# Kernel tuning notes

Hardware: AMD Instinct MI355X
Metric: run time of the kernel (lower is better)

Reference implementation:

```python
import jax, jax.numpy as jnp
import numpy as np
from jax import lax

D = 384      # embd_d
L = 4        # num_blocks
B = 64
SHW, THW = 24, 12
NS, NT = SHW * SHW, THW * THW   # 576, 144
EPS = 1e-5


def _ln(x, g, b):
    mu = jnp.mean(x, axis=-1, keepdims=True)
    var = jnp.mean(jnp.square(x - mu), axis=-1, keepdims=True)
    return (x - mu) * lax.rsqrt(var + EPS) * g + b


def setup_inputs() -> dict:
    key = jax.random.key(0)
    ks = iter(jax.random.split(key, 64))
    f32 = jnp.float32
    def nrm(shape, s=0.02):
        return jax.random.normal(next(ks), shape, dtype=f32) * s
    inp = {
        'search': jax.random.normal(next(ks), (B, NS, D), dtype=f32),
        'target': jax.random.normal(next(ks), (B, NT, D), dtype=f32),
        # learned tokens / positional params
        'cls': nrm((1, 1, D), 1.0),
        'search_pos': nrm((1, NS, D), 0.5),
        'target_pos': nrm((1, NT, D), 0.5),
        # stacked per-block params [L, ...]
        'ln1_g': jnp.ones((L, D), f32), 'ln1_b': jnp.zeros((L, D), f32),
        'Wq': nrm((L, D, D)), 'bq': jnp.zeros((L, D), f32),
        'Wk': nrm((L, D, D)), 'bk': jnp.zeros((L, D), f32),
        'Wv': nrm((L, D, D)), 'bv': jnp.zeros((L, D), f32),
        'ln2_g': jnp.ones((L, D), f32), 'ln2_b': jnp.zeros((L, D), f32),
        'W1': nrm((L, D, 2 * D)), 'b1': jnp.zeros((L, 2 * D), f32),
        'W2': nrm((L, 2 * D, D)), 'b2': jnp.zeros((L, D), f32),
        # head
        'lnf_g': jnp.ones((D,), f32), 'lnf_b': jnp.zeros((D,), f32),
        'Wl1': nrm((D, D)), 'bl1': jnp.zeros((D,), f32),
        'Wl2': nrm((D, 1)), 'bl2': jnp.zeros((1,), f32),
    }
    return inp


def reference(search, target, cls, search_pos, target_pos,
              ln1_g, ln1_b, Wq, bq, Wk, bk, Wv, bv,
              ln2_g, ln2_b, W1, b1, W2, b2,
              lnf_g, lnf_b, Wl1, bl1, Wl2, bl2):
    scale = D ** (-0.5)  # note: full embed dim, as in source
    x = jnp.concatenate([
        jnp.broadcast_to(cls, (B, 1, D)),
        search + search_pos,
        target + target_pos,
    ], axis=1)  # [B, 1+Ns+Nt, D]

    def block(x, p):
        l1g, l1b, wq, bq_, wk, bk_, wv, bv_, l2g, l2b, w1, b1_, w2, b2_ = p
        y = _ln(x, l1g, l1b)
        q = y @ wq + bq_
        k = y @ wk + bk_
        v = y @ wv + bv_
        attn = jax.nn.softmax(jnp.einsum('bid,bjd->bij', q, k) * scale, axis=-1)
        x = x + jnp.einsum('bij,bjd->bid', attn, v)
        h = _ln(x, l2g, l2b)
        x = x + (jax.nn.gelu(h @ w1 + b1_, approximate=False) @ w2 + b2_)
        return x, None

    x, _ = lax.scan(block, x, (ln1_g, ln1_b, Wq, bq, Wk, bk, Wv, bv,
                               ln2_g, ln2_b, W1, b1, W2, b2))
    h = _ln(x[:, 0], lnf_g, lnf_b)          # cls token [B, D]
    h = jax.nn.relu(h @ Wl1 + bl1)
    return h @ Wl2 + bl2                     # [B, 1]
```

## Files before the change

### kernel.cpp

```cpp
#include <hip/hip_runtime.h>
#include <hip/hip_bf16.h>
#include <math.h>

#define DD 384
#define NBATCH 64
#define NSEQ 721
#define NROWS (NBATCH*NSEQ)
#define NLAYER 4
#define VTW 736

typedef __bf16 bf16_t;
typedef __bf16 bf16x8 __attribute__((ext_vector_type(8)));
typedef float  f32x4  __attribute__((ext_vector_type(4)));

static __device__ __forceinline__ void split_bf16(float v, bf16_t& h, bf16_t& l) {
    h = (bf16_t)v;
    l = (bf16_t)(v - (float)h);
}
static __device__ __forceinline__ bf16x8 bzero8() {
    bf16x8 v = {(bf16_t)0.f,(bf16_t)0.f,(bf16_t)0.f,(bf16_t)0.f,
                (bf16_t)0.f,(bf16_t)0.f,(bf16_t)0.f,(bf16_t)0.f};
    return v;
}
static __device__ __forceinline__ void gload16(const void* g, void* l) {
    __builtin_amdgcn_global_load_lds(
        (const __attribute__((address_space(1))) unsigned int*)g,
        (__attribute__((address_space(3))) unsigned int*)l, 16, 0, 0);
}
static __device__ __forceinline__ int xcd_swz(int nwg) {
    int orig = blockIdx.x;
    int q = nwg >> 3, r = nwg & 7;
    int xcd = orig & 7, within = orig >> 3;
    int base = (xcd < r) ? xcd*(q+1) : r*(q+1) + (xcd - r)*q;
    return base + within;
}
static __device__ __forceinline__ void ln_from_partials(const float* ss, const float* ss2,
                                                        int row, float& mu, float& rstd) {
    float s = 0.f, q2 = 0.f;
    #pragma unroll
    for (int k = 0; k < 6; ++k) { s += ss[k*NROWS + row]; q2 += ss2[k*NROWS + row]; }
    mu = s * (1.f/DD);
    float var = q2 * (1.f/DD) - mu*mu;
    rstd = rsqrtf(var + 1e-5f);
}

__global__ __launch_bounds__(256) void build_x_kernel(const float* __restrict__ search,
                               const float* __restrict__ target,
                               const float* __restrict__ cls,
                               const float* __restrict__ spos,
                               const float* __restrict__ tpos,
                               bf16_t* __restrict__ xh, bf16_t* __restrict__ xl,
                               float* __restrict__ wss, float* __restrict__ wss2) {
    int wave = threadIdx.x >> 6, lane = threadIdx.x & 63;
    int row = blockIdx.x * 4 + wave;
    if (row >= NROWS) return;
    int b = row / NSEQ, n = row % NSEQ;
    float s = 0.f, q2 = 0.f;
    #pragma unroll
    for (int i = 0; i < 6; ++i) {
        int d = lane + 64*i;
        float val;
        if (n == 0)        val = cls[d];
        else if (n <= 576) val = search[((size_t)b*576 + (n-1))*DD + d] + spos[(size_t)(n-1)*DD + d];
        else               val = target[((size_t)b*144 + (n-577))*DD + d] + tpos[(size_t)(n-577)*DD + d];
        bf16_t h, l;
        split_bf16(val, h, l);
        xh[(size_t)row*DD + d] = h;
        xl[(size_t)row*DD + d] = l;
        s += val; q2 += val*val;
    }
    #pragma unroll
    for (int m = 1; m < 64; m <<= 1) { s += __shfl_xor(s, m); q2 += __shfl_xor(q2, m); }
    if (lane == 0) {
        wss[row] = s; wss2[row] = q2;
        #pragma unroll
        for (int k = 1; k < 6; ++k) { wss[k*NROWS + row] = 0.f; wss2[k*NROWS + row] = 0.f; }
    }
}

__global__ void transpose_split_kernel(const float* __restrict__ src,
                                       const float* __restrict__ g,
                                       bf16_t* __restrict__ dh,
                                       bf16_t* __restrict__ dl,
                                       int K, int N) {
    int idx = blockIdx.x * blockDim.x + threadIdx.x;
    if (idx >= K*N) return;
    int k = idx / N, n = idx % N;
    float v = src[idx];
    if (g) v *= g[k];
    bf16_t h, l;
    split_bf16(v, h, l);
    dh[(size_t)n*K + k] = h;
    dl[(size_t)n*K + k] = l;
}

__global__ void colsum_kernel(const float* __restrict__ W, const float* __restrict__ g,
                              const float* __restrict__ b, const float* __restrict__ bias,
                              float* __restrict__ c1, float* __restrict__ c2,
                              int K, int N, int outStride, int outOff) {
    int l = blockIdx.y;
    int n = blockIdx.x * 256 + threadIdx.x;
    if (n >= N) return;
    const float* Wl = W + (size_t)l*K*N;
    const float* gl = g + (size_t)l*K;
    const float* bl = b + (size_t)l*K;
    float s1 = 0.f, s2 = 0.f;
    for (int k = 0; k < K; ++k) {
        float w = Wl[(size_t)k*N + n];
        s1 = fmaf(gl[k], w, s1);
        s2 = fmaf(bl[k], w, s2);
    }
    c1[(size_t)l*outStride + outOff + n] = s1;
    c2[(size_t)l*outStride + outOff + n] = s2 + bias[(size_t)l*N + n];
}

static __device__ __forceinline__ void gemm_core(
        const bf16_t* __restrict__ ah, const bf16_t* __restrict__ al,
        const bf16_t* __restrict__ bh, const bf16_t* __restrict__ bl,
        bf16_t (&ls)[32][64][8],
        int m0, int n0, int K, f32x4 (&acc)[4][4]) {
    int t = threadIdx.x;
    int w = t >> 6, lane = t & 63;
    int c = lane & 15, g = lane >> 4;
    int wr = w >> 1, wc = w & 1;
    const bf16_t* src0 = (w==0) ? ah : (w==1) ? al : (w==2) ? bh : bl;
    int base_rc = (w < 2) ? m0 : n0;
    const bf16_t* srcbase = src0 + (size_t)(base_rc + c)*K + 8*g;

    int ksteps = K >> 5;
    for (int kt = 0; kt < ksteps; ++kt) {
        int k0 = kt << 5;
        __syncthreads();
        #pragma unroll
        for (int i = 0; i < 8; ++i)
            gload16(srcbase + (size_t)(16*i)*K + k0, &ls[w*8 + i][0][0]);
        __syncthreads();
        bf16x8 af_h[4], af_l[4], bf_h[4], bf_l[4];
        #pragma unroll
        for (int i = 0; i < 4; ++i) {
            af_h[i] = *(const bf16x8*)&ls[     4*wr + i][lane][0];
            af_l[i] = *(const bf16x8*)&ls[ 8 + 4*wr + i][lane][0];
            bf_h[i] = *(const bf16x8*)&ls[16 + 4*wc + i][lane][0];
            bf_l[i] = *(const bf16x8*)&ls[24 + 4*wc + i][lane][0];
        }
        #pragma unroll
        for (int i = 0; i < 4; ++i)
            #pragma unroll
            for (int j = 0; j < 4; ++j) {
                acc[i][j] = __builtin_amdgcn_mfma_f32_16x16x32_bf16(af_h[i], bf_h[j], acc[i][j], 0,0,0);
                acc[i][j] = __builtin_amdgcn_mfma_f32_16x16x32_bf16(af_h[i], bf_l[j], acc[i][j], 0,0,0);
                acc[i][j] = __builtin_amdgcn_mfma_f32_16x16x32_bf16(af_l[i], bf_h[j], acc[i][j], 0,0,0);
            }
    }
}

__global__ __launch_bounds__(256, 4) void gemm_qkv(
        const bf16_t* __restrict__ ah, const bf16_t* __restrict__ al,
        const bf16_t* __restrict__ bh, const bf16_t* __restrict__ bl,
        const float* __restrict__ ss, const float* __restrict__ ss2,
        const float* __restrict__ c1, const float* __restrict__ c2,
        bf16_t* __restrict__ qout, bf16_t* __restrict__ kout,
        bf16_t* __restrict__ vth,
        int nwg) {
    __shared__ __align__(16) bf16_t ls[32][64][8];
    int wgid = xcd_swz(nwg);
    int mt = wgid / 9, n0 = (wgid % 9) * 128;
    int blb = mt / 6;
    int tok_base = (mt % 6) * 128;
    int m0d = blb*NSEQ + tok_base;
    f32x4 zero4 = {0.f,0.f,0.f,0.f};
    f32x4 acc[4][4];
    #pragma unroll
    for (int i = 0; i < 4; ++i)
        #pragma unroll
        for (int j = 0; j < 4; ++j) acc[i][j] = zero4;
    gemm_core(ah, al, bh, bl, ls, m0d, n0, DD, acc);

    int t = threadIdx.x, w = t >> 6, lane = t & 63;
    int c = lane & 15, g = lane >> 4;
    int wr = w >> 1, wc = w & 1;
    float rmu[16], rrs[16];
    #pragma unroll
    for (int i = 0; i < 4; ++i)
        #pragma unroll
        for (int r = 0; r < 4; ++r) {
            int tok = tok_base + 64*wr + 16*i + 4*g + r;
            float mu = 0.f, rstd = 1.f;
            if (tok < NSEQ) ln_from_partials(ss, ss2, blb*NSEQ + tok, mu, rstd);
            rmu[i*4+r] = mu; rrs[i*4+r] = rstd;
        }
    int seg = n0 / 384;
    bf16_t* LST = &ls[0][0][0];
    if (seg < 2) {
        bf16_t* outb = (seg == 0) ? qout : kout;
        int segoff = seg * 384;
        __syncthreads();
        #pragma unroll
        for (int j = 0; j < 4; ++j) {
            int nl = 64*wc + 16*j + c;
            float C1 = c1[n0 + nl], C2 = c2[n0 + nl];
            #pragma unroll
            for (int i = 0; i < 4; ++i)
                #pragma unroll
                for (int r = 0; r < 4; ++r) {
                    int rl = 64*wr + 16*i + 4*g + r;
                    float val = rrs[i*4+r]*(acc[i][j][r] - rmu[i*4+r]*C1) + C2;
                    LST[rl*128 + (nl ^ ((rl & 15) << 3))] = (bf16_t)val;
                }
        }
        __syncthreads();
        #pragma unroll
        for (int p = 0; p < 8; ++p) {
            int chunk = t + 256*p;
            int rl = chunk >> 4;
            int nl0 = (chunk & 15) * 8;
            int tok = tok_base + rl;
            if (tok >= NSEQ) continue;
            uint4 v = *(const uint4*)&LST[rl*128 + (nl0 ^ ((rl & 15) << 3))];
            *(uint4*)(outb + (size_t)(blb*NSEQ + tok)*DD + (n0 - segoff) + nl0) = v;
        }
    } else {
        int vbase = n0 - 768;
        __syncthreads();
        #pragma unroll
        for (int j = 0; j < 4; ++j) {
            int d = 64*wc + 16*j + c;
            float C1 = c1[n0 + d], C2 = c2[n0 + d];
            #pragma unroll
            for (int i = 0; i < 4; ++i)
                #pragma unroll
                for (int r = 0; r < 4; ++r) {
                    int tokl = 64*wr + 16*i + 4*g + r;
                    float val = rrs[i*4+r]*(acc[i][j][r] - rmu[i*4+r]*C1) + C2;
                    if (tok_base + tokl >= NSEQ) val = 0.f;
                    LST[d*128 + (tokl ^ ((d & 15) << 3))] = (bf16_t)val;
                }
        }
        __syncthreads();
        #pragma unroll
        for (int p = 0; p < 8; ++p) {
            int chunk = t + 256*p;
            int d = chunk >> 4;
            int tok0 = (chunk & 15) * 8;
            int tg = tok_base + tok0;
            if (tg + 8 > VTW) continue;
            uint4 v = *(const uint4*)&LST[d*128 + (tok0 ^ ((d & 15) << 3))];
            *(uint4*)(vth + ((size_t)(blb*DD + vbase + d))*VTW + tg) = v;
        }
    }
}

template<int EPI, int NT>
__global__ __launch_bounds__(256, 4) void gemm_mfma(
        const bf16_t* __restrict__ ah, const bf16_t* __restrict__ al,
        const bf16_t* __restrict__ bh, const bf16_t* __restrict__ bl,
        const float* __restrict__ ss, const float* __restrict__ ss2,
        const float* __restrict__ c1, const float* __restrict__ c2,
        const float* __restrict__ bias,
        const bf16_t* __restrict__ resh, const bf16_t* __restrict__ resl,
        bf16_t* __restrict__ o1, bf16_t* __restrict__ o2,
        float* __restrict__ wss, float* __restrict__ wss2,
        int M, int N, int K, int nwg) {
    __shared__ __align__(16) bf16_t ls[32][64][8];
    int wgid = xcd_swz(nwg);
    int m0 = (wgid / NT) * 128, n0 = (wgid % NT) * 128;
    f32x4 zero4 = {0.f,0.f,0.f,0.f};
    f32x4 acc[4][4];
    #pragma unroll
    for (int i = 0; i < 4; ++i)
        #pragma unroll
        for (int j = 0; j < 4; ++j) acc[i][j] = zero4;
    gemm_core(ah, al, bh, bl, ls, m0, n0, K, acc);

    int t = threadIdx.x, w = t >> 6, lane = t & 63;
    int c = lane & 15, g = lane >> 4;
    int wr = w >> 1, wc = w & 1;

    if (EPI == 2) {
        float rmu[16], rrs[16];
        #pragma unroll
        for (int i = 0; i < 4; ++i)
            #pragma unroll
            for (int r = 0; r < 4; ++r) {
                int row = m0 + 64*wr + 16*i + 4*g + r;
                float mu = 0.f, rstd = 1.f;
                if (row < M) ln_from_partials(ss, ss2, row, mu, rstd);
                rmu[i*4+r] = mu; rrs[i*4+r] = rstd;
            }
        #pragma unroll
        for (int j = 0; j < 4; ++j) {
            int n = n0 + 64*wc + 16*j + c;
            float C1 = c1[n], C2 = c2[n];
            #pragma unroll
            for (int i = 0; i < 4; ++i) {
                int rbase = m0 + 64*wr + 16*i + 4*g;
                #pragma unroll
                for (int r = 0; r < 4; ++r) {
                    int row = rbase + r;
                    if (row >= M) continue;
                    float val = rrs[i*4+r]*(acc[i][j][r] - rmu[i*4+r]*C1) + C2;
                    val = 0.5f*val*(1.0f + erff(val*0.70710678118654752f));
                    bf16_t h, l;
                    split_bf16(val, h, l);
                    size_t o = (size_t)row*N + n;
                    o1[o] = h;
                    o2[o] = l;
                }
            }
        }
    } else {
        int slot = (wgid % NT) + 3*wc;
        #pragma unroll
        for (int i = 0; i < 4; ++i)
            #pragma unroll
            for (int r = 0; r < 4; ++r) {
                int row = m0 + 64*wr + 16*i + 4*g + r;
                if (row >= M) continue;
                float s = 0.f, q2 = 0.f;
                #pragma unroll
                for (int j = 0; j < 4; ++j) {
                    int n = n0 + 64*wc + 16*j + c;
                    size_t o = (size_t)row*N + n;
                    float val = acc[i][j][r] + bias[n] + (float)resh[o] + (float)resl[o];
                    bf16_t h, l;
                    split_bf16(val, h, l);
                    o1[o] = h;
                    o2[o] = l;
                    s += val; q2 += val*val;
                }
                #pragma unroll
                for (int m = 1; m < 16; m <<= 1) { s += __shfl_xor(s, m); q2 += __shfl_xor(q2, m); }
                if (c == 0) {
                    wss[slot*NROWS + row] = s;
                    wss2[slot*NROWS + row] = q2;
                }
            }
    }
}

__global__ __launch_bounds__(256, 2) void attn_mfma(
        const bf16_t* __restrict__ qh, const bf16_t* __restrict__ kh,
        const bf16_t* __restrict__ vth,
        bf16_t* __restrict__ xh, bf16_t* __restrict__ xl,
        float* __restrict__ wss, float* __restrict__ wss2, int nwg) {
    __shared__ __align__(16) char smem[49152];
    bf16_t* kf = (bf16_t*)smem;
    char* vhp = smem + 24576;

    int t = threadIdx.x, w = t >> 6, lane = t & 63;
    int c = lane & 15, g = lane >> 4;
    int wgid = xcd_swz(nwg);
    int bl_ = wgid / 12;
    int q0 = (wgid % 12) * 64;
    size_t bb = (size_t)bl_ * NSEQ;
    int qrow = q0 + 16*w + c;
    bool qok = (qrow < NSEQ);
    const float scale = 0.05103103630798287f;
    int vswz = (c ^ (c >> 2)) & 3;
    int dma_dd  = lane >> 2;
    int dma_kv8 = (lane & 3) ^ ((dma_dd ^ (dma_dd >> 2)) & 3);

    bf16x8 qf[12];
    #pragma unroll
    for (int ks = 0; ks < 12; ++ks) {
        if (qok) qf[ks] = *(const bf16x8*)(qh + (bb + qrow)*DD + 32*ks + 8*g);
        else     qf[ks] = bzero8();
    }

    f32x4 zero4 = {0.f,0.f,0.f,0.f};
    f32x4 oacc[24];
    #pragma unroll
    for (int i = 0; i < 24; ++i) oacc[i] = zero4;
    float m_run = -1e30f, l_run = 0.f;

    #pragma unroll
    for (int i = 0; i < 6; ++i) {
        int s = i*4 + w;
        int ks = s >> 1, mf = s & 1;
        gload16(kh + (bb + (size_t)(16*mf + c))*DD + 32*ks + 8*g, kf + s*512);
    }

    for (int kt = 0; kt < 23; ++kt) {
        int kv0 = kt * 32;
        asm volatile("s_waitcnt vmcnt(0)" ::: "memory");
        __builtin_amdgcn_s_barrier();
        #pragma unroll
        for (int i = 0; i < 6; ++i) {
            int s = i*4 + w;
            size_t gro = ((size_t)(bl_*DD + 16*s + dma_dd))*VTW + kv0 + 8*dma_kv8;
            gload16(vth + gro, (bf16_t*)vhp + s*512);
        }
        f32x4 sacc[2];
        sacc[0] = zero4; sacc[1] = zero4;
        #pragma unroll
        for (int ks = 0; ks < 12; ++ks) {
            bf16x8 a0 = *(const bf16x8*)(kf + ((size_t)(2*ks+0)*64 + lane)*8);
            bf16x8 a1 = *(const bf16x8*)(kf + ((size_t)(2*ks+1)*64 + lane)*8);
            sacc[0] = __builtin_amdgcn_mfma_f32_16x16x32_bf16(a0, qf[ks], sacc[0], 0,0,0);
            sacc[1] = __builtin_amdgcn_mfma_f32_16x16x32_bf16(a1, qf[ks], sacc[1], 0,0,0);
        }
        float p[2][4];
        float mx = -1e30f;
        #pragma unroll
        for (int mf = 0; mf < 2; ++mf)
            #pragma unroll
            for (int r = 0; r < 4; ++r) {
                float sv = sacc[mf][r] * scale;
                int kv = kv0 + 16*mf + 4*g + r;
                if (kv >= NSEQ) sv = -1e30f;
                p[mf][r] = sv;
                mx = fmaxf(mx, sv);
            }
        mx = fmaxf(mx, __shfl_xor(mx, 16));
        mx = fmaxf(mx, __shfl_xor(mx, 32));
        bool skip = __all(mx <= m_run + 8.f);
        float m_new = skip ? m_run : fmaxf(m_run, mx);
        float psum = 0.f;
        #pragma unroll
        for (int mf = 0; mf < 2; ++mf)
            #pragma unroll
            for (int r = 0; r < 4; ++r) {
                float pv = __expf(p[mf][r] - m_new);
                p[mf][r] = pv;
                psum += pv;
            }
        psum += __shfl_xor(psum, 16);
        psum += __shfl_xor(psum, 32);
        if (!skip) {
            float corr = __expf(m_run - m_new);
            l_run = l_run * corr + psum;
            #pragma unroll
            for (int i = 0; i < 24; ++i) oacc[i] *= corr;
            m_run = m_new;
        } else {
            l_run += psum;
        }
        bf16x8 ph, pl;
        #pragma unroll
        for (int mf = 0; mf < 2; ++mf)
            #pragma unroll
            for (int r = 0; r < 4; ++r) {
                bf16_t hh, ll;
                split_bf16(p[mf][r], hh, ll);
                ph[mf*4 + r] = hh;
                pl[mf*4 + r] = ll;
            }
        asm volatile("s_waitcnt vmcnt(0)" ::: "memory");
        __builtin_amdgcn_s_barrier();
        if (kt + 1 < 23) {
            int kv0n = kv0 + 32;
            #pragma unroll
            for (int i = 0; i < 6; ++i) {
                int s = i*4 + w;
                int ks = s >> 1, mf = s & 1;
                gload16(kh + (bb + (size_t)(kv0n + 16*mf + c))*DD + 32*ks + 8*g, kf + s*512);
            }
        }
        #pragma unroll
        for (int mf = 0; mf < 24; ++mf) {
            int dr = 16*mf + c;
            const char* vb = vhp + dr*64;
            int o0 = ((((g>>1)     ^ vswz) << 4) | (8*(g&1)));
            int o1 = (((2 + (g>>1)) ^ vswz) << 4) | (8*(g&1));
            union { uint2 u[2]; bf16x8 v; } va;
            va.u[0] = *(const uint2*)(vb + o0);
            va.u[1] = *(const uint2*)(vb + o1);
            oacc[mf] = __builtin_amdgcn_mfma_f32_16x16x32_bf16(va.v, ph, oacc[mf], 0,0,0);
            oacc[mf] = __builtin_amdgcn_mfma_f32_16x16x32_bf16(va.v, pl, oacc[mf], 0,0,0);
        }
    }
    float inv = 1.f / l_run;
    float s = 0.f, q2 = 0.f;
    if (qok) {
        bf16_t* xhr = xh + (bb + qrow)*DD;
        bf16_t* xlr = xl + (bb + qrow)*DD;
        #pragma unroll
        for (int mf = 0; mf < 24; ++mf)
            #pragma unroll
            for (int r = 0; r < 4; ++r) {
                int d = 16*mf + 4*g + r;
                float xv = (float)xhr[d] + (float)xlr[d] + oacc[mf][r]*inv;
                bf16_t h, l;
                split_bf16(xv, h, l);
                xhr[d] = h;
                xlr[d] = l;
                s += xv; q2 += xv*xv;
            }
    }
    s += __shfl_xor(s, 16);  q2 += __shfl_xor(q2, 16);
    s += __shfl_xor(s, 32);  q2 += __shfl_xor(q2, 32);
    if (qok && g == 0) {
        int rowL = bl_*NSEQ + qrow;
        wss[rowL] = s; wss2[rowL] = q2;
        #pragma unroll
        for (int k = 1; k < 6; ++k) { wss[k*NROWS + rowL] = 0.f; wss2[k*NROWS + rowL] = 0.f; }
    }
}

__global__ __launch_bounds__(384) void head_kernel(const bf16_t* __restrict__ xh,
    const bf16_t* __restrict__ xl,
    const float* __restrict__ g, const float* __restrict__ bb,
    const float* __restrict__ Wl1, const float* __restrict__ bl1,
    const float* __restrict__ Wl2, const float* __restrict__ bl2,
    float* __restrict__ outp) {
    __shared__ float yv[384];
    __shared__ float r1[6], r2[6], r3[6];
    int b = blockIdx.x, t = threadIdx.x;
    size_t o = (size_t)b*NSEQ*DD + t;
    float v = (float)xh[o] + (float)xl[o];
    float s = v;
    #pragma unroll
    for (int m = 1; m < 64; m <<= 1) s += __shfl_xor(s, m);
    if ((t & 63) == 0) r1[t>>6] = s;
    __syncthreads();
    float mu = (r1[0]+r1[1]+r1[2]+r1[3]+r1[4]+r1[5]) * (1.f/384.f);
    float dd = v - mu;
    float sq = dd*dd;
    #pragma unroll
    for (int m = 1; m < 64; m <<= 1) sq += __shfl_xor(sq, m);
    if ((t & 63) == 0) r2[t>>6] = sq;
    __syncthreads();
    float var = (r2[0]+r2[1]+r2[2]+r2[3]+r2[4]+r2[5]) * (1.f/384.f);
    float rstd = rsqrtf(var + 1e-5f);
    yv[t] = dd*rstd*g[t] + bb[t];
    __syncthreads();
    float acc = bl1[t];
    for (int d2 = 0; d2 < 384; d2++) acc = fmaf(yv[d2], Wl1[d2*384 + t], acc);
    acc = fmaxf(acc, 0.f);
    float oo = acc * Wl2[t];
    #pragma unroll
    for (int m = 1; m < 64; m <<= 1) oo += __shfl_xor(oo, m);
    if ((t & 63) == 0) r3[t>>6] = oo;
    __syncthreads();
    if (t == 0) outp[b] = r3[0]+r3[1]+r3[2]+r3[3]+r3[4]+r3[5] + bl2[0];
}

extern "C" void kernel_launch(void* const* d_in, const int* in_sizes, int n_in,
                              void* d_out, int out_size, void* d_ws, size_t ws_size,
                              hipStream_t stream) {
    const float* search = (const float*)d_in[0];
    const float* target = (const float*)d_in[1];
    const float* cls    = (const float*)d_in[2];
    const float* spos   = (const float*)d_in[3];
    const float* tpos   = (const float*)d_in[4];
    const float* ln1_g  = (const float*)d_in[5];
    const float* ln1_b  = (const float*)d_in[6];
    const float* Wq     = (const float*)d_in[7];
    const float* bq     = (const float*)d_in[8];
    const float* Wk     = (const float*)d_in[9];
    const float* bk     = (const float*)d_in[10];
    const float* Wv     = (const float*)d_in[11];
    const float* bv     = (const float*)d_in[12];
    const float* ln2_g  = (const float*)d_in[13];
    const float* ln2_b  = (const float*)d_in[14];
    const float* W1     = (const float*)d_in[15];
    const float* b1     = (const float*)d_in[16];
    const float* W2     = (const float*)d_in[17];
    const float* b2     = (const float*)d_in[18];
    const float* lnf_g  = (const float*)d_in[19];
    const float* lnf_b  = (const float*)d_in[20];
    const float* Wl1    = (const float*)d_in[21];
    const float* bl1    = (const float*)d_in[22];
    const float* Wl2    = (const float*)d_in[23];
    const float* bl2    = (const float*)d_in[24];

    size_t off = 0;
    char* base = (char*)d_ws;
    auto alloc = [&](size_t bytes) -> void* {
        void* p = base + off;
        off += (bytes + 255) & ~(size_t)255;
        return p;
    };

    bf16_t* xh = (bf16_t*)alloc((size_t)NROWS * DD * 2);
    bf16_t* xl = (bf16_t*)alloc((size_t)NROWS * DD * 2);
    float* ssum  = (float*)alloc((size_t)6*NROWS*4);
    float* ssum2 = (float*)alloc((size_t)6*NROWS*4);

    const int SQKV = 1152*DD;
    const int SM = DD*768;
    bf16_t* wqkvh = (bf16_t*)alloc((size_t)4*SQKV*2);
    bf16_t* wqkvl = (bf16_t*)alloc((size_t)4*SQKV*2);
    bf16_t* w1h = (bf16_t*)alloc((size_t)4*SM*2);
    bf16_t* w1l = (bf16_t*)alloc((size_t)4*SM*2);
    bf16_t* w2h = (bf16_t*)alloc((size_t)4*SM*2);
    bf16_t* w2l = (bf16_t*)alloc((size_t)4*SM*2);
    float* cqkv1 = (float*)alloc((size_t)4*1152*4);
    float* cqkv2 = (float*)alloc((size_t)4*1152*4);
    float* cm11  = (float*)alloc((size_t)4*768*4);
    float* cm12  = (float*)alloc((size_t)4*768*4);

    const size_t qB  = (size_t)NSEQ*DD*2;
    const size_t mB  = (size_t)NSEQ*768*2;
    const size_t perB = 2*mB;
    size_t avail = (ws_size > off + 262144) ? (ws_size - off - 262144) : 0;
    int G = (int)(avail / perB);
    if (G > NBATCH) G = NBATCH;
    if (G < 1) G = 1;

    char* U = (char*)alloc(perB * G);
    bf16_t* qhB  = (bf16_t*)U;
    bf16_t* khB  = (bf16_t*)(U + qB*G);
    bf16_t* vth  = (bf16_t*)(U + 2*qB*G);
    bf16_t* midh = (bf16_t*)U;
    bf16_t* midl = (bf16_t*)(U + mB*G);

    build_x_kernel<<<(NROWS+3)/4, 256, 0, stream>>>(search, target, cls, spos, tpos,
                                                    xh, xl, ssum, ssum2);

    const int SQ = DD*DD;
    for (int l = 0; l < NLAYER; ++l) {
        bf16_t* dsth = wqkvh + (size_t)l*SQKV;
        bf16_t* dstl = wqkvl + (size_t)l*SQKV;
        transpose_split_kernel<<<(SQ+255)/256, 256, 0, stream>>>(Wq + (size_t)l*SQ, ln1_g + l*DD, dsth,          dstl,          DD, DD);
        transpose_split_kernel<<<(SQ+255)/256, 256, 0, stream>>>(Wk + (size_t)l*SQ, ln1_g + l*DD, dsth + 384*DD, dstl + 384*DD, DD, DD);
        transpose_split_kernel<<<(SQ+255)/256, 256, 0, stream>>>(Wv + (size_t)l*SQ, ln1_g + l*DD, dsth + 768*DD, dstl + 768*DD, DD, DD);
        transpose_split_kernel<<<(SM+255)/256, 256, 0, stream>>>(W1 + (size_t)l*SM, ln2_g + l*DD, w1h + (size_t)l*SM, w1l + (size_t)l*SM, DD, 768);
        transpose_split_kernel<<<(SM+255)/256, 256, 0, stream>>>(W2 + (size_t)l*SM, nullptr,      w2h + (size_t)l*SM, w2l + (size_t)l*SM, 768, DD);
    }
    colsum_kernel<<<dim3(2, NLAYER), 256, 0, stream>>>(Wq, ln1_g, ln1_b, bq, cqkv1, cqkv2, DD, DD, 1152, 0);
    colsum_kernel<<<dim3(2, NLAYER), 256, 0, stream>>>(Wk, ln1_g, ln1_b, bk, cqkv1, cqkv2, DD, DD, 1152, 384);
    colsum_kernel<<<dim3(2, NLAYER), 256, 0, stream>>>(Wv, ln1_g, ln1_b, bv, cqkv1, cqkv2, DD, DD, 1152, 768);
    colsum_kernel<<<dim3(3, NLAYER), 256, 0, stream>>>(W1, ln2_g, ln2_b, b1, cm11, cm12, DD, 768, 768, 0);

    for (int l = 0; l < NLAYER; ++l) {
        for (int b0 = 0; b0 < NBATCH; b0 += G) {
            int cb = (NBATCH - b0 < G) ? (NBATCH - b0) : G;
            int Mc = cb * NSEQ;
            bf16_t* xch = xh + (size_t)b0 * NSEQ * DD;
            bf16_t* xcl = xl + (size_t)b0 * NSEQ * DD;
            float* ssc  = ssum  + (size_t)b0 * NSEQ;
            float* ssc2 = ssum2 + (size_t)b0 * NSEQ;
            int mtiles = (Mc + 127)/128;
            int nwgQKV = 9*6*cb, nwgM1 = 6*mtiles, nwgM2 = 3*mtiles, nwgA = 12*cb;

            gemm_qkv<<<nwgQKV, 256, 0, stream>>>(xch, xcl,
                    wqkvh + (size_t)l*SQKV, wqkvl + (size_t)l*SQKV,
                    ssc, ssc2, cqkv1 + l*1152, cqkv2 + l*1152,
                    qhB, khB, vth, nwgQKV);
            attn_mfma<<<nwgA, 256, 0, stream>>>(qhB, khB, vth, xch, xcl,
                    ssc, ssc2, nwgA);
            gemm_mfma<2,6><<<nwgM1, 256, 0, stream>>>(xch, xcl,
                    w1h + (size_t)l*SM, w1l + (size_t)l*SM,
                    ssc, ssc2, cm11 + l*768, cm12 + l*768, nullptr,
                    nullptr, nullptr, midh, midl, nullptr, nullptr, Mc, 768, DD, nwgM1);
            gemm_mfma<3,3><<<nwgM2, 256, 0, stream>>>(midh, midl,
                    w2h + (size_t)l*SM, w2l + (size_t)l*SM,
                    nullptr, nullptr, nullptr, nullptr, b2 + l*DD,
                    xch, xcl, xch, xcl, ssc, ssc2, Mc, DD, 768, nwgM2);
        }
    }
    head_kernel<<<NBATCH, 384, 0, stream>>>(xh, xl, lnf_g, lnf_b, Wl1, bl1, Wl2, bl2, (float*)d_out);
}
```

Measured before the change: 3.237 ms.

## Drop activation low-part MFMAs in QKV/MLP1 and stage epilogue stores through LDS

```diff
diff --git a/kernel.cpp b/kernel.cpp
--- a/kernel.cpp
+++ b/kernel.cpp
@@ -114,7 +114,7 @@
     c2[(size_t)l*outStride + outOff + n] = s2 + bias[(size_t)l*N + n];
 }
 
-static __device__ __forceinline__ void gemm_core(
+static __device__ __forceinline__ void gemm_core3(
         const bf16_t* __restrict__ ah, const bf16_t* __restrict__ al,
         const bf16_t* __restrict__ bh, const bf16_t* __restrict__ bl,
         bf16_t (&ls)[32][64][8],
@@ -154,8 +154,48 @@
     }
 }
 
+static __device__ __forceinline__ void gemm_core2(
+        const bf16_t* __restrict__ ah,
+        const bf16_t* __restrict__ bh, const bf16_t* __restrict__ bl,
+        bf16_t (&ls)[32][64][8],
+        int m0, int n0, int K, f32x4 (&acc)[4][4]) {
+    int t = threadIdx.x;
+    int w = t >> 6, lane = t & 63;
+    int c = lane & 15, g = lane >> 4;
+    int wr = w >> 1, wc = w & 1;
+
+    int ksteps = K >> 5;
+    for (int kt = 0; kt < ksteps; ++kt) {
+        int k0 = kt << 5;
+        __syncthreads();
+        #pragma unroll
+        for (int i = 0; i < 6; ++i) {
+            int s = w*6 + i;
+            const bf16_t* src = (s < 8) ? ah : (s < 16) ? bh : bl;
+            int base = (s < 8) ? m0 : n0;
+            int row = base + (s & 7)*16 + c;
+            gload16(src + (size_t)row*K + k0 + 8*g, &ls[s][0][0]);
+        }
+        __syncthreads();
+        bf16x8 af[4], bfh[4], bfl[4];
+        #pragma unroll
+        for (int i = 0; i < 4; ++i) {
+            af[i]  = *(const bf16x8*)&ls[     4*wr + i][lane][0];
+            bfh[i] = *(const bf16x8*)&ls[ 8 + 4*wc + i][lane][0];
+            bfl[i] = *(const bf16x8*)&ls[16 + 4*wc + i][lane][0];
+        }
+        #pragma unroll
+        for (int i = 0; i < 4; ++i)
+            #pragma unroll
+            for (int j = 0; j < 4; ++j) {
+                acc[i][j] = __builtin_amdgcn_mfma_f32_16x16x32_bf16(af[i], bfh[j], acc[i][j], 0,0,0);
+                acc[i][j] = __builtin_amdgcn_mfma_f32_16x16x32_bf16(af[i], bfl[j], acc[i][j], 0,0,0);
+            }
+    }
+}
+
 __global__ __launch_bounds__(256, 4) void gemm_qkv(
-        const bf16_t* __restrict__ ah, const bf16_t* __restrict__ al,
+        const bf16_t* __restrict__ ah,
         const bf16_t* __restrict__ bh, const bf16_t* __restrict__ bl,
         const float* __restrict__ ss, const float* __restrict__ ss2,
         const float* __restrict__ c1, const float* __restrict__ c2,
@@ -174,7 +214,7 @@
     for (int i = 0; i < 4; ++i)
         #pragma unroll
         for (int j = 0; j < 4; ++j) acc[i][j] = zero4;
-    gemm_core(ah, al, bh, bl, ls, m0d, n0, DD, acc);
+    gemm_core2(ah, bh, bl, ls, m0d, n0, DD, acc);
 
     int t = threadIdx.x, w = t >> 6, lane = t & 63;
     int c = lane & 15, g = lane >> 4;
@@ -250,91 +290,179 @@
     }
 }
 
-template<int EPI, int NT>
-__global__ __launch_bounds__(256, 4) void gemm_mfma(
-        const bf16_t* __restrict__ ah, const bf16_t* __restrict__ al,
+__global__ __launch_bounds__(256, 4) void gemm_m1(
+        const bf16_t* __restrict__ ah,
         const bf16_t* __restrict__ bh, const bf16_t* __restrict__ bl,
         const float* __restrict__ ss, const float* __restrict__ ss2,
         const float* __restrict__ c1, const float* __restrict__ c2,
+        bf16_t* __restrict__ o1, bf16_t* __restrict__ o2,
+        int M, int nwg) {
+    __shared__ __align__(16) bf16_t ls[32][64][8];
+    int wgid = xcd_swz(nwg);
+    int m0 = (wgid / 6) * 128, n0 = (wgid % 6) * 128;
+    f32x4 zero4 = {0.f,0.f,0.f,0.f};
+    f32x4 acc[4][4];
+    #pragma unroll
+    for (int i = 0; i < 4; ++i)
+        #pragma unroll
+        for (int j = 0; j < 4; ++j) acc[i][j] = zero4;
+    gemm_core2(ah, bh, bl, ls, m0, n0, DD, acc);
+
+    int t = threadIdx.x, w = t >> 6, lane = t & 63;
+    int c = lane & 15, g = lane >> 4;
+    int wr = w >> 1, wc = w & 1;
+    float rmu[16], rrs[16];
+    #pragma unroll
+    for (int i = 0; i < 4; ++i)
+        #pragma unroll
+        for (int r = 0; r < 4; ++r) {
+            int row = m0 + 64*wr + 16*i + 4*g + r;
+            float mu = 0.f, rstd = 1.f;
+            if (row < M) ln_from_partials(ss, ss2, row, mu, rstd);
+            rmu[i*4+r] = mu; rrs[i*4+r] = rstd;
+        }
+    bf16_t* LST = &ls[0][0][0];
+    __syncthreads();
+    #pragma unroll
+    for (int j = 0; j < 4; ++j) {
+        int nl = 64*wc + 16*j + c;
+        float C1 = c1[n0 + nl], C2 = c2[n0 + nl];
+        #pragma unroll
+        for (int i = 0; i < 4; ++i)
+            #pragma unroll
+            for (int r = 0; r < 4; ++r) {
+                int rl = 64*wr + 16*i + 4*g + r;
+                float val = rrs[i*4+r]*(acc[i][j][r] - rmu[i*4+r]*C1) + C2;
+                val = 0.5f*val*(1.0f + erff(val*0.70710678118654752f));
+                acc[i][j][r] = val;
+                LST[rl*128 + (nl ^ ((rl & 15) << 3))] = (bf16_t)val;
+            }
+    }
+    __syncthreads();
+    #pragma unroll
+    for (int p = 0; p < 8; ++p) {
+        int chunk = t + 256*p;
+        int rl = chunk >> 4;
+        int nl0 = (chunk & 15) * 8;
+        int row = m0 + rl;
+        if (row >= M) continue;
+        uint4 v = *(const uint4*)&LST[rl*128 + (nl0 ^ ((rl & 15) << 3))];
+        *(uint4*)(o1 + (size_t)row*768 + n0 + nl0) = v;
+    }
+    __syncthreads();
+    #pragma unroll
+    for (int j = 0; j < 4; ++j) {
+        int nl = 64*wc + 16*j + c;
+        #pragma unroll
+        for (int i = 0; i < 4; ++i)
+            #pragma unroll
+            for (int r = 0; r < 4; ++r) {
+                int rl = 64*wr + 16*i + 4*g + r;
+                float val = acc[i][j][r];
+                bf16_t h, l;
+                split_bf16(val, h, l);
+                LST[rl*128 + (nl ^ ((rl & 15) << 3))] = l;
+            }
+    }
+    __syncthreads();
+    #pragma unroll
+    for (int p = 0; p < 8; ++p) {
+        int chunk = t + 256*p;
+        int rl = chunk >> 4;
+        int nl0 = (chunk & 15) * 8;
+        int row = m0 + rl;
+        if (row >= M) continue;
+        uint4 v = *(const uint4*)&LST[rl*128 + (nl0 ^ ((rl & 15) << 3))];
+        *(uint4*)(o2 + (size_t)row*768 + n0 + nl0) = v;
+    }
+}
+
+__global__ __launch_bounds__(256, 4) void gemm_m2(
+        const bf16_t* __restrict__ ah, const bf16_t* __restrict__ al,
+        const bf16_t* __restrict__ bh, const bf16_t* __restrict__ bl,
         const float* __restrict__ bias,
         const bf16_t* __restrict__ resh, const bf16_t* __restrict__ resl,
         bf16_t* __restrict__ o1, bf16_t* __restrict__ o2,
         float* __restrict__ wss, float* __restrict__ wss2,
-        int M, int N, int K, int nwg) {
+        int M, int nwg) {
     __shared__ __align__(16) bf16_t ls[32][64][8];
     int wgid = xcd_swz(nwg);
-    int m0 = (wgid / NT) * 128, n0 = (wgid % NT) * 128;
+    int m0 = (wgid / 3) * 128, n0 = (wgid % 3) * 128;
     f32x4 zero4 = {0.f,0.f,0.f,0.f};
     f32x4 acc[4][4];
     #pragma unroll
     for (int i = 0; i < 4; ++i)
         #pragma unroll
         for (int j = 0; j < 4; ++j) acc[i][j] = zero4;
-    gemm_core(ah, al, bh, bl, ls, m0, n0, K, acc);
+    gemm_core3(ah, al, bh, bl, ls, m0, n0, 768, acc);
 
     int t = threadIdx.x, w = t >> 6, lane = t & 63;
     int c = lane & 15, g = lane >> 4;
     int wr = w >> 1, wc = w & 1;
-
-    if (EPI == 2) {
-        float rmu[16], rrs[16];
-        #pragma unroll
-        for (int i = 0; i < 4; ++i)
-            #pragma unroll
-            for (int r = 0; r < 4; ++r) {
-                int row = m0 + 64*wr + 16*i + 4*g + r;
-                float mu = 0.f, rstd = 1.f;
-                if (row < M) ln_from_partials(ss, ss2, row, mu, rstd);
-                rmu[i*4+r] = mu; rrs[i*4+r] = rstd;
-            }
-        #pragma unroll
-        for (int j = 0; j < 4; ++j) {
-            int n = n0 + 64*wc + 16*j + c;
-            float C1 = c1[n], C2 = c2[n];
-            #pragma unroll
-            for (int i = 0; i < 4; ++i) {
-                int rbase = m0 + 64*wr + 16*i + 4*g;
-                #pragma unroll
-                for (int r = 0; r < 4; ++r) {
-                    int row = rbase + r;
-                    if (row >= M) continue;
-                    float val = rrs[i*4+r]*(acc[i][j][r] - rmu[i*4+r]*C1) + C2;
-                    val = 0.5f*val*(1.0f + erff(val*0.70710678118654752f));
-                    bf16_t h, l;
-                    split_bf16(val, h, l);
-                    size_t o = (size_t)row*N + n;
-                    o1[o] = h;
-                    o2[o] = l;
-                }
-            }
-        }
-    } else {
-        int slot = (wgid % NT) + 3*wc;
-        #pragma unroll
-        for (int i = 0; i < 4; ++i)
-            #pragma unroll
-            for (int r = 0; r < 4; ++r) {
-                int row = m0 + 64*wr + 16*i + 4*g + r;
-                if (row >= M) continue;
-                float s = 0.f, q2 = 0.f;
+    int slot = (wgid % 3) + 3*wc;
+    bf16_t* LST = &ls[0][0][0];
+    __syncthreads();
+    #pragma unroll
+    for (int i = 0; i < 4; ++i)
+        #pragma unroll
+        for (int r = 0; r < 4; ++r) {
+            int rl = 64*wr + 16*i + 4*g + r;
+            int row = m0 + rl;
+            float s = 0.f, q2 = 0.f;
+            if (row < M) {
                 #pragma unroll
                 for (int j = 0; j < 4; ++j) {
-                    int n = n0 + 64*wc + 16*j + c;
-                    size_t o = (size_t)row*N + n;
-                    float val = acc[i][j][r] + bias[n] + (float)resh[o] + (float)resl[o];
-                    bf16_t h, l;
-                    split_bf16(val, h, l);
-                    o1[o] = h;
-                    o2[o] = l;
+                    int nl = 64*wc + 16*j + c;
+                    size_t o = (size_t)row*DD + n0 + nl;
+                    float val = acc[i][j][r] + bias[n0 + nl] + (float)resh[o] + (float)resl[o];
+                    acc[i][j][r] = val;
+                    LST[rl*128 + (nl ^ ((rl & 15) << 3))] = (bf16_t)val;
                     s += val; q2 += val*val;
                 }
-                #pragma unroll
-                for (int m = 1; m < 16; m <<= 1) { s += __shfl_xor(s, m); q2 += __shfl_xor(q2, m); }
-                if (c == 0) {
-                    wss[slot*NROWS + row] = s;
-                    wss2[slot*NROWS + row] = q2;
-                }
-            }
+            }
+            #pragma unroll
+            for (int m = 1; m < 16; m <<= 1) { s += __shfl_xor(s, m); q2 += __shfl_xor(q2, m); }
+            if (row < M && c == 0) {
+                wss[slot*NROWS + row] = s;
+                wss2[slot*NROWS + row] = q2;
+            }
+        }
+    __syncthreads();
+    #pragma unroll
+    for (int p = 0; p < 8; ++p) {
+        int chunk = t + 256*p;
+        int rl = chunk >> 4;
+        int nl0 = (chunk & 15) * 8;
+        int row = m0 + rl;
+        if (row >= M) continue;
+        uint4 v = *(const uint4*)&LST[rl*128 + (nl0 ^ ((rl & 15) << 3))];
+        *(uint4*)(o1 + (size_t)row*DD + n0 + nl0) = v;
+    }
+    __syncthreads();
+    #pragma unroll
+    for (int i = 0; i < 4; ++i)
+        #pragma unroll
+        for (int r = 0; r < 4; ++r) {
+            int rl = 64*wr + 16*i + 4*g + r;
+            if (m0 + rl >= M) continue;
+            #pragma unroll
+            for (int j = 0; j < 4; ++j) {
+                int nl = 64*wc + 16*j + c;
+                bf16_t h, l;
+                split_bf16(acc[i][j][r], h, l);
+                LST[rl*128 + (nl ^ ((rl & 15) << 3))] = l;
+            }
+        }
+    __syncthreads();
+    #pragma unroll
+    for (int p = 0; p < 8; ++p) {
+        int chunk = t + 256*p;
+        int rl = chunk >> 4;
+        int nl0 = (chunk & 15) * 8;
+        int row = m0 + rl;
+        if (row >= M) continue;
+        uint4 v = *(const uint4*)&LST[rl*128 + (nl0 ^ ((rl & 15) << 3))];
+        *(uint4*)(o2 + (size_t)row*DD + n0 + nl0) = v;
     }
 }
 
@@ -634,20 +762,19 @@
             int mtiles = (Mc + 127)/128;
             int nwgQKV = 9*6*cb, nwgM1 = 6*mtiles, nwgM2 = 3*mtiles, nwgA = 12*cb;
 
-            gemm_qkv<<<nwgQKV, 256, 0, stream>>>(xch, xcl,
+            gemm_qkv<<<nwgQKV, 256, 0, stream>>>(xch,
                     wqkvh + (size_t)l*SQKV, wqkvl + (size_t)l*SQKV,
                     ssc, ssc2, cqkv1 + l*1152, cqkv2 + l*1152,
                     qhB, khB, vth, nwgQKV);
             attn_mfma<<<nwgA, 256, 0, stream>>>(qhB, khB, vth, xch, xcl,
                     ssc, ssc2, nwgA);
-            gemm_mfma<2,6><<<nwgM1, 256, 0, stream>>>(xch, xcl,
+            gemm_m1<<<nwgM1, 256, 0, stream>>>(xch,
                     w1h + (size_t)l*SM, w1l + (size_t)l*SM,
-                    ssc, ssc2, cm11 + l*768, cm12 + l*768, nullptr,
-                    nullptr, nullptr, midh, midl, nullptr, nullptr, Mc, 768, DD, nwgM1);
-            gemm_mfma<3,3><<<nwgM2, 256, 0, stream>>>(midh, midl,
+                    ssc, ssc2, cm11 + l*768, cm12 + l*768,
+                    midh, midl, Mc, nwgM1);
+            gemm_m2<<<nwgM2, 256, 0, stream>>>(midh, midl,
                     w2h + (size_t)l*SM, w2l + (size_t)l*SM,
-                    nullptr, nullptr, nullptr, nullptr, b2 + l*DD,
-                    xch, xcl, xch, xcl, ssc, ssc2, Mc, DD, 768, nwgM2);
+                    b2 + l*DD, xch, xcl, xch, xcl, ssc, ssc2, Mc, nwgM2);
         }
     }
     head_kernel<<<NBATCH, 384, 0, stream>>>(xh, xl, lnf_g, lnf_b, Wl1, bl1, Wl2, bl2, (float*)d_out);
```

New measurement: 3.676 ms. 13.6% more time.
